# Optimization experiments

Measured on AMD Instinct MI355X. Metric: run time of the kernel, lower is better.

## Reference

```python
import jax, jax.numpy as jnp
import numpy as np

N = 2048      # number of ROIs
C = 1024      # in_channels == inter_channels
G = 16        # groups
D = C // G    # per-group dim = 64


def _bbox_overlaps(b1, b2):
    # mmdet-1.x IoU with +1 pixel convention; b1:(N,4), b2:(M,4)
    area1 = (b1[:, 2] - b1[:, 0] + 1) * (b1[:, 3] - b1[:, 1] + 1)  # (N,)
    area2 = (b2[:, 2] - b2[:, 0] + 1) * (b2[:, 3] - b2[:, 1] + 1)  # (M,)
    lt = jnp.maximum(b1[:, None, :2], b2[None, :, :2])             # (N,M,2)
    rb = jnp.minimum(b1[:, None, 2:], b2[None, :, 2:])             # (N,M,2)
    wh = jnp.clip(rb - lt + 1, 0)
    inter = wh[..., 0] * wh[..., 1]                                # (N,M)
    return inter / (area1[:, None] + area2[None, :] - inter)


def setup_inputs() -> dict:
    key = jax.random.key(0)
    ks = jax.random.split(key, 9)
    in_x = jax.random.normal(ks[0], (N, C), dtype=jnp.float32)
    # valid boxes: [batch_idx, x1, y1, x2, y2]
    xy = jax.random.uniform(ks[1], (N, 2), minval=0.0, maxval=800.0)
    wh = jax.random.uniform(ks[2], (N, 2), minval=8.0, maxval=200.0)
    rois = jnp.concatenate([jnp.zeros((N, 1)), xy, xy + wh], axis=1).astype(jnp.float32)
    s = 1.0 / np.sqrt(C)
    W0 = jax.random.normal(ks[3], (C, C), dtype=jnp.float32) * s
    b0 = jnp.zeros((C,), dtype=jnp.float32)
    W1 = jax.random.normal(ks[4], (C, C), dtype=jnp.float32) * s
    b1 = jnp.zeros((C,), dtype=jnp.float32)
    # grouped 1x1 conv: per group maps C channels -> D channels
    Wout = jax.random.normal(ks[5], (G, D, C), dtype=jnp.float32) * s
    bout = jnp.zeros((C,), dtype=jnp.float32)
    return {"in_x": in_x, "rois": rois, "W0": W0, "b0": b0, "W1": W1,
            "b1": b1, "Wout": Wout, "bout": bout}


def reference(in_x, rois, W0, b0, W1, b1, Wout, bout):
    # self-attention path: in_ref_x = in_x, ref_rois = rois
    # embed convs are pre-activation (relu -> 1x1 conv), shared for x and ref_x
    def embed(v):
        v = jax.nn.relu(v) @ W0.T + b0
        v = jax.nn.relu(v) @ W1.T + b1
        return v
    x = embed(in_x)                      # (N, C)
    ref_x = x                            # shared convs, same input
    xg = x.reshape(N, G, D)
    rg = ref_x.reshape(N, G, D)
    scores = jnp.einsum('ngd,mgd->ngm', xg, rg) / jnp.sqrt(jnp.float32(D))  # (N,G,N)
    ious = _bbox_overlaps(rois[:, 1:], rois[:, 1:])                          # (N,N)
    scores = scores + jnp.log(ious[:, None, :] + 1e-6)
    attn = jax.nn.softmax(scores, axis=2)                                    # (N,G,N)
    y = jnp.einsum('ngm,mc->ngc', attn, in_x)                                # (N,G,C)
    out = jnp.einsum('ngc,goc->ngo', y, Wout).reshape(N, C) + bout           # (N,C)
    return out
```

## Files before the change

### kernel.cpp

```cpp
#include <hip/hip_runtime.h>
#include <math.h>

constexpr int NROI = 2048;
constexpr int CDIM = 1024;
constexpr int NG   = 16;
constexpr int DH   = 64;

typedef __attribute__((ext_vector_type(8))) short short8;
typedef __attribute__((ext_vector_type(4))) float floatx4;

#define MFMA_BF16(a, b, c) __builtin_amdgcn_mfma_f32_16x16x32_bf16((a), (b), (c), 0, 0, 0)

__device__ __forceinline__ short f2bf(float f) {
  unsigned u = __float_as_uint(f);
  unsigned r = 0x7fffu + ((u >> 16) & 1u);
  return (short)((u + r) >> 16);
}
__device__ __forceinline__ unsigned pack2(float a, float b) {
  return (unsigned)(unsigned short)f2bf(a) | ((unsigned)(unsigned short)f2bf(b) << 16);
}

typedef __attribute__((address_space(1))) void GV;
typedef __attribute__((address_space(3))) void LV;
__device__ __forceinline__ void gl2lds16(const void* g, void* l) {
  __builtin_amdgcn_global_load_lds((GV*)g, (LV*)l, 16, 0, 0);
}

__device__ __forceinline__ short8 brelu(short8 v) {
  union { short8 s; unsigned u[4]; } x; x.s = v;
#pragma unroll
  for (int i = 0; i < 4; ++i) {
    unsigned m = (x.u[i] >> 15) & 0x10001u;
    x.u[i] &= ~(m * 0xFFFFu);
  }
  return x.s;
}

__global__ __launch_bounds__(256) void convert_kernel(
    const float* __restrict__ in_x, const float* __restrict__ W0,
    const float* __restrict__ W1, const float* __restrict__ Wout,
    short* __restrict__ xin_b, short* __restrict__ W0b,
    short* __restrict__ W1b, short* __restrict__ Woutb)
{
  const int i = blockIdx.x * 256 + threadIdx.x;
  {
    const float4 v = ((const float4*)in_x)[i];
    uint2 u; u.x = pack2(v.x, v.y); u.y = pack2(v.z, v.w);
    ((uint2*)xin_b)[i] = u;
  }
  if (i < 262144) {
    float4 v = ((const float4*)W0)[i];
    uint2 u; u.x = pack2(v.x, v.y); u.y = pack2(v.z, v.w);
    ((uint2*)W0b)[i] = u;
    v = ((const float4*)W1)[i];
    u.x = pack2(v.x, v.y); u.y = pack2(v.z, v.w);
    ((uint2*)W1b)[i] = u;
    v = ((const float4*)Wout)[i];
    u.x = pack2(v.x, v.y); u.y = pack2(v.z, v.w);
    ((uint2*)Woutb)[i] = u;
  }
}

__global__ __launch_bounds__(256) void iou_kernel(const float* __restrict__ rois,
                                                  unsigned short* __restrict__ biasb)
{
  const int q = blockIdx.y;
  const int k = blockIdx.x * 256 + threadIdx.x;
  const float qx1 = rois[q * 5 + 1], qy1 = rois[q * 5 + 2];
  const float qx2 = rois[q * 5 + 3], qy2 = rois[q * 5 + 4];
  const float qa = (qx2 - qx1 + 1.f) * (qy2 - qy1 + 1.f);
  const float kx1 = rois[k * 5 + 1], ky1 = rois[k * 5 + 2];
  const float kx2 = rois[k * 5 + 3], ky2 = rois[k * 5 + 4];
  const float ka = (kx2 - kx1 + 1.f) * (ky2 - ky1 + 1.f);
  float iw = fminf(qx2, kx2) - fmaxf(qx1, kx1) + 1.f;
  float ih = fminf(qy2, ky2) - fmaxf(qy1, ky1) + 1.f;
  iw = fmaxf(iw, 0.f); ih = fmaxf(ih, 0.f);
  const float inter = iw * ih;
  const float iou = inter / (qa + ka - inter);
  biasb[(size_t)q * NROI + k] = (unsigned short)f2bf(iou + 1e-6f);
}

__global__ __launch_bounds__(256) void gemm_fusedA(
    const short* __restrict__ A, const short* __restrict__ BW0,
    const short* __restrict__ BWout, const float* __restrict__ b0,
    short* __restrict__ t0b, short* __restrict__ zT)
{
  __shared__ short As[8 * 512];
  __shared__ short Bs[8 * 512];
  const int isW0 = blockIdx.x < 16;
  const int col0 = (blockIdx.x & 15) * 64;
  const short* B = isW0 ? BW0 : BWout;
  const int t = threadIdx.x, w = t >> 6, lane = t & 63;
  const int wm = w >> 1, wn = w & 1;
  const int row0 = blockIdx.y * 64;
  const int rlo = lane & 15, khi = (lane >> 4) * 8;

  floatx4 acc[2][2];
#pragma unroll
  for (int i = 0; i < 2; ++i)
#pragma unroll
    for (int j = 0; j < 2; ++j) acc[i][j] = (floatx4){0.f, 0.f, 0.f, 0.f};

  for (int k0 = 0; k0 < CDIM; k0 += 64) {
    __syncthreads();
#pragma unroll
    for (int kh = 0; kh < 2; ++kh) {
      gl2lds16(A + (size_t)(row0 + w * 16 + rlo) * CDIM + k0 + kh * 32 + khi,
               &As[(w * 2 + kh) * 512]);
      gl2lds16(B + (size_t)(col0 + w * 16 + rlo) * CDIM + k0 + kh * 32 + khi,
               &Bs[(w * 2 + kh) * 512]);
    }
    __syncthreads();
#pragma unroll
    for (int kh = 0; kh < 2; ++kh) {
      short8 a0 = *(const short8*)&As[((wm * 2 + 0) * 2 + kh) * 512 + lane * 8];
      short8 a1 = *(const short8*)&As[((wm * 2 + 1) * 2 + kh) * 512 + lane * 8];
      if (isW0) { a0 = brelu(a0); a1 = brelu(a1); }
      const short8 b0f = *(const short8*)&Bs[((wn * 2 + 0) * 2 + kh) * 512 + lane * 8];
      const short8 b1f = *(const short8*)&Bs[((wn * 2 + 1) * 2 + kh) * 512 + lane * 8];
      acc[0][0] = MFMA_BF16(a0, b0f, acc[0][0]);
      acc[0][1] = MFMA_BF16(a0, b1f, acc[0][1]);
      acc[1][0] = MFMA_BF16(a1, b0f, acc[1][0]);
      acc[1][1] = MFMA_BF16(a1, b1f, acc[1][1]);
    }
  }

  const int colL = lane & 15, qq = lane >> 4;
  float bj[2] = {0.f, 0.f};
  if (isW0) {
    bj[0] = b0[col0 + wn * 32 + colL];
    bj[1] = b0[col0 + wn * 32 + 16 + colL];
  }
#pragma unroll
  for (int i = 0; i < 2; ++i)
#pragma unroll
    for (int j = 0; j < 2; ++j)
#pragma unroll
      for (int r = 0; r < 4; ++r) {
        const int row = row0 + wm * 32 + i * 16 + qq * 4 + r;
        const int cc  = col0 + wn * 32 + j * 16 + colL;
        const short bv = f2bf(acc[i][j][r] + bj[j]);
        if (isW0) t0b[(size_t)row * CDIM + cc] = bv;
        else      zT[(size_t)cc * NROI + row] = bv;
      }
}

__global__ __launch_bounds__(256) void gemm_relu_nt(
    const short* __restrict__ A, const short* __restrict__ B,
    const float* __restrict__ bias, short* __restrict__ C)
{
  __shared__ short As[8 * 512];
  __shared__ short Bs[8 * 512];
  const int t = threadIdx.x, w = t >> 6, lane = t & 63;
  const int wm = w >> 1, wn = w & 1;
  const int row0 = blockIdx.y * 64, col0 = blockIdx.x * 64;
  const int rlo = lane & 15, khi = (lane >> 4) * 8;

  floatx4 acc[2][2];
#pragma unroll
  for (int i = 0; i < 2; ++i)
#pragma unroll
    for (int j = 0; j < 2; ++j) acc[i][j] = (floatx4){0.f, 0.f, 0.f, 0.f};

  for (int k0 = 0; k0 < CDIM; k0 += 64) {
    __syncthreads();
#pragma unroll
    for (int kh = 0; kh < 2; ++kh) {
      gl2lds16(A + (size_t)(row0 + w * 16 + rlo) * CDIM + k0 + kh * 32 + khi,
               &As[(w * 2 + kh) * 512]);
      gl2lds16(B + (size_t)(col0 + w * 16 + rlo) * CDIM + k0 + kh * 32 + khi,
               &Bs[(w * 2 + kh) * 512]);
    }
    __syncthreads();
#pragma unroll
    for (int kh = 0; kh < 2; ++kh) {
      short8 a0 = *(const short8*)&As[((wm * 2 + 0) * 2 + kh) * 512 + lane * 8];
      short8 a1 = *(const short8*)&As[((wm * 2 + 1) * 2 + kh) * 512 + lane * 8];
      a0 = brelu(a0); a1 = brelu(a1);
      const short8 b0f = *(const short8*)&Bs[((wn * 2 + 0) * 2 + kh) * 512 + lane * 8];
      const short8 b1f = *(const short8*)&Bs[((wn * 2 + 1) * 2 + kh) * 512 + lane * 8];
      acc[0][0] = MFMA_BF16(a0, b0f, acc[0][0]);
      acc[0][1] = MFMA_BF16(a0, b1f, acc[0][1]);
      acc[1][0] = MFMA_BF16(a1, b0f, acc[1][0]);
      acc[1][1] = MFMA_BF16(a1, b1f, acc[1][1]);
    }
  }

  const int colL = lane & 15, qq = lane >> 4;
  float bj[2];
  bj[0] = bias[col0 + wn * 32 + colL];
  bj[1] = bias[col0 + wn * 32 + 16 + colL];
#pragma unroll
  for (int i = 0; i < 2; ++i)
#pragma unroll
    for (int j = 0; j < 2; ++j)
#pragma unroll
      for (int r = 0; r < 4; ++r) {
        const int row = row0 + wm * 32 + i * 16 + qq * 4 + r;
        const int cc  = col0 + wn * 32 + j * 16 + colL;
        C[(size_t)row * CDIM + cc] = f2bf(acc[i][j][r] + bj[j]);
      }
}

__global__ __launch_bounds__(512) void attn_split(
    const short* __restrict__ Xb,
    const short* __restrict__ ZTb,
    const unsigned short* __restrict__ biasb,
    float* __restrict__ O0, short* __restrict__ O1,
    float* __restrict__ lsums)
{
  const int g  = blockIdx.y;
  const int n0 = blockIdx.x * 128;
  const int sp = blockIdx.z;
  const int mbase = sp * 1024;
  const int t = threadIdx.x, w = t >> 6, lane = t & 63;
  const int col = lane & 15, qq = lane >> 4;
  const int t16 = (w >> 1) * 16, h32 = (w & 1) * 32;
  const int rlo = lane & 15, khi = (lane >> 4) * 8;

  __shared__ short Kf[2][8 * 512];
  __shared__ short Vf[2][8 * 512];
  __shared__ short Pf[8 * 1024];

  const size_t qoff = (size_t)(n0 + w * 16 + col) * CDIM + g * DH;
  const short8 qf0 = *(const short8*)(Xb + qoff + qq * 8);
  const short8 qf1 = *(const short8*)(Xb + qoff + 32 + qq * 8);

  floatx4 oc[4];
#pragma unroll
  for (int dt = 0; dt < 4; ++dt) oc[dt] = (floatx4){0.f, 0.f, 0.f, 0.f};
  float lsum[4] = {0.f, 0.f, 0.f, 0.f};

  const int qrow0 = n0 + w * 16 + qq * 4;

  uint2 bbc[4], bbn[4];
#pragma unroll
  for (int ct = 0; ct < 4; ++ct)
    bbc[ct] = *(const uint2*)(biasb + (size_t)(mbase + ct * 16 + col) * NROI + qrow0);

  gl2lds16(Xb + (size_t)(mbase + t16 + rlo) * CDIM + g * DH + h32 + khi, &Kf[0][w * 512]);
  gl2lds16(ZTb + (size_t)(g * DH + t16 + rlo) * NROI + mbase + h32 + khi, &Vf[0][w * 512]);
  __syncthreads();

  for (int it = 0; it < 16; ++it) {
    const int p = it & 1;
    if (it < 15) {
      const int m1 = mbase + (it + 1) * 64;
      gl2lds16(Xb + (size_t)(m1 + t16 + rlo) * CDIM + g * DH + h32 + khi,
               &Kf[1 - p][w * 512]);
      gl2lds16(ZTb + (size_t)(g * DH + t16 + rlo) * NROI + m1 + h32 + khi,
               &Vf[1 - p][w * 512]);
#pragma unroll
      for (int ct = 0; ct < 4; ++ct)
        bbn[ct] = *(const uint2*)(biasb + (size_t)(m1 + ct * 16 + col) * NROI + qrow0);
    }

    floatx4 sc[4];
#pragma unroll
    for (int ct = 0; ct < 4; ++ct) {
      const short8 b0 = *(const short8*)&Kf[p][(ct * 2 + 0) * 512 + lane * 8];
      const short8 b1 = *(const short8*)&Kf[p][(ct * 2 + 1) * 512 + lane * 8];
      floatx4 z4 = (floatx4){0.f, 0.f, 0.f, 0.f};
      z4 = MFMA_BF16(qf0, b0, z4);
      z4 = MFMA_BF16(qf1, b1, z4);
      sc[ct] = z4;
    }

#pragma unroll
    for (int ct = 0; ct < 4; ++ct) {
      const unsigned ux = bbc[ct].x, uy = bbc[ct].y;
      sc[ct][0] = __expf(sc[ct][0] * 0.125f) * __uint_as_float(ux << 16);
      sc[ct][1] = __expf(sc[ct][1] * 0.125f) * __uint_as_float(ux & 0xFFFF0000u);
      sc[ct][2] = __expf(sc[ct][2] * 0.125f) * __uint_as_float(uy << 16);
      sc[ct][3] = __expf(sc[ct][3] * 0.125f) * __uint_as_float(uy & 0xFFFF0000u);
    }
#pragma unroll
    for (int r = 0; r < 4; ++r)
      lsum[r] += sc[0][r] + sc[1][r] + sc[2][r] + sc[3][r];

    {
      short* pw = &Pf[w * 1024];
#pragma unroll
      for (int ct = 0; ct < 4; ++ct) {
        const int key = ct * 16 + col;
        const int base = (key >> 5) * 512 + (key & 7);
#pragma unroll
        for (int r = 0; r < 4; ++r) {
          const int dl = (4 * qq + r) + ((key >> 3) & 3) * 16;
          pw[base + dl * 8] = f2bf(sc[ct][r]);
        }
      }
      const short8 pa0 = *(const short8*)&pw[0 * 512 + lane * 8];
      const short8 pa1 = *(const short8*)&pw[1 * 512 + lane * 8];
#pragma unroll
      for (int dt = 0; dt < 4; ++dt) {
        const short8 v0 = *(const short8*)&Vf[p][(dt * 2 + 0) * 512 + lane * 8];
        const short8 v1 = *(const short8*)&Vf[p][(dt * 2 + 1) * 512 + lane * 8];
        oc[dt] = MFMA_BF16(pa0, v0, oc[dt]);
        oc[dt] = MFMA_BF16(pa1, v1, oc[dt]);
      }
    }
    __syncthreads();
#pragma unroll
    for (int ct = 0; ct < 4; ++ct) bbc[ct] = bbn[ct];
  }

#pragma unroll
  for (int r = 0; r < 4; ++r) {
    float s = lsum[r];
    s += __shfl_xor(s, 1); s += __shfl_xor(s, 2);
    s += __shfl_xor(s, 4); s += __shfl_xor(s, 8);
    lsum[r] = s;
  }
  if (col == 0) {
#pragma unroll
    for (int r = 0; r < 4; ++r)
      lsums[sp * (NG * NROI) + g * NROI + qrow0 + r] = lsum[r];
  }
  if (sp == 0) {
#pragma unroll
    for (int dt = 0; dt < 4; ++dt)
#pragma unroll
      for (int r = 0; r < 4; ++r)
        O0[(size_t)(qrow0 + r) * CDIM + g * DH + dt * 16 + col] = oc[dt][r];
  } else {
#pragma unroll
    for (int dt = 0; dt < 4; ++dt)
#pragma unroll
      for (int r = 0; r < 4; ++r)
        O1[(size_t)(qrow0 + r) * CDIM + g * DH + dt * 16 + col] = f2bf(oc[dt][r]);
  }
}

__global__ __launch_bounds__(256) void merge_kernel(
    const float* __restrict__ O0, const short* __restrict__ O1,
    const float* __restrict__ lsums, const float* __restrict__ bout,
    float* __restrict__ Out)
{
  const int i = blockIdx.x * 256 + threadIdx.x;
  const int base = i * 4, q = base >> 10, c = base & 1023, g = c >> 6;
  const float l = lsums[g * NROI + q] + lsums[NG * NROI + g * NROI + q];
  const float linv = 1.f / l;
  const float4 o0 = ((const float4*)O0)[i];
  const uint2 o1 = ((const uint2*)O1)[i];
  const float4 bo = *(const float4*)(bout + c);
  float4 o;
  o.x = (o0.x + __uint_as_float(o1.x << 16))          * linv + bo.x;
  o.y = (o0.y + __uint_as_float(o1.x & 0xFFFF0000u))  * linv + bo.y;
  o.z = (o0.z + __uint_as_float(o1.y << 16))          * linv + bo.z;
  o.w = (o0.w + __uint_as_float(o1.y & 0xFFFF0000u))  * linv + bo.w;
  ((float4*)Out)[i] = o;
}

extern "C" void kernel_launch(void* const* d_in, const int* in_sizes, int n_in,
                              void* d_out, int out_size, void* d_ws, size_t ws_size,
                              hipStream_t stream) {
  const float* in_x = (const float*)d_in[0];
  const float* rois = (const float*)d_in[1];
  const float* W0   = (const float*)d_in[2];
  const float* b0   = (const float*)d_in[3];
  const float* W1   = (const float*)d_in[4];
  const float* b1   = (const float*)d_in[5];
  const float* Wout = (const float*)d_in[6];
  const float* bout = (const float*)d_in[7];
  char* w8 = (char*)d_ws;

  short* xin_b = (short*)w8;
  short* W0b   = (short*)(w8 + (4u << 20));
  short* Woutb = (short*)(w8 + (6u << 20));
  unsigned short* biasb = (unsigned short*)(w8 + (4u << 20));
  short* zT    = (short*)(w8 + (12u << 20));
  short* O1    = (short*)(w8 + (16u << 20));
  short* W1b   = (short*)(w8 + (20u << 20));
  float* lsums = (float*)(w8 + (20u << 20));
  short* xb  = xin_b;
  short* t0b = (short*)d_out;
  float* O0  = (float*)d_out;

  convert_kernel<<<2048, 256, 0, stream>>>(in_x, W0, W1, Wout,
                                           xin_b, W0b, W1b, Woutb);
  gemm_fusedA<<<dim3(32, 32), 256, 0, stream>>>(xin_b, W0b, Woutb, b0, t0b, zT);
  iou_kernel<<<dim3(NROI / 256, NROI), 256, 0, stream>>>(rois, biasb);
  gemm_relu_nt<<<dim3(16, 32), 256, 0, stream>>>(t0b, W1b, b1, xb);
  attn_split<<<dim3(NROI / 128, NG, 2), 512, 0, stream>>>(xb, zT, biasb, O0, O1, lsums);
  merge_kernel<<<2048, 256, 0, stream>>>(O0, O1, lsums, bout, (float*)d_out);
}
```

Before: 201.1 us.

## Fuse IoU into convert, enlarge first GEMM tiles, drop attention split and merge

The IoU computation is folded into the conversion kernel and now stores log(iou) in bf16, so the attention exponent becomes a single fmaf+exp. The first GEMM moves from 64x64 to 128x128 tiles, and the transposed Wout-projection stores are packed into 64-bit writes. The attention kernel no longer splits the key range into two halves: it loops over all 2048 keys, normalizes and adds the bias in its own epilogue, and the merge kernel is removed. This saves launches and the intermediate O0/O1/lsum traffic, but halves the attention grid (256 blocks), which can lower occupancy on a many-CU device. It also quantizes P with truncation instead of rounding.

```diff
diff --git a/kernel.cpp b/kernel.cpp
--- a/kernel.cpp
+++ b/kernel.cpp
@@ -16,6 +16,9 @@
   unsigned r = 0x7fffu + ((u >> 16) & 1u);
   return (short)((u + r) >> 16);
 }
+__device__ __forceinline__ short f2bf_rtz(float f) {
+  return (short)(__float_as_uint(f) >> 16);
+}
 __device__ __forceinline__ unsigned pack2(float a, float b) {
   return (unsigned)(unsigned short)f2bf(a) | ((unsigned)(unsigned short)f2bf(b) << 16);
 }
@@ -36,113 +39,132 @@
   return x.s;
 }
 
-__global__ __launch_bounds__(256) void convert_kernel(
+__global__ __launch_bounds__(256) void conv_iou(
     const float* __restrict__ in_x, const float* __restrict__ W0,
     const float* __restrict__ W1, const float* __restrict__ Wout,
+    const float* __restrict__ rois,
     short* __restrict__ xin_b, short* __restrict__ W0b,
-    short* __restrict__ W1b, short* __restrict__ Woutb)
+    short* __restrict__ W1b, short* __restrict__ Woutb,
+    unsigned short* __restrict__ biasln)
 {
-  const int i = blockIdx.x * 256 + threadIdx.x;
-  {
-    const float4 v = ((const float4*)in_x)[i];
-    uint2 u; u.x = pack2(v.x, v.y); u.y = pack2(v.z, v.w);
-    ((uint2*)xin_b)[i] = u;
-  }
-  if (i < 262144) {
-    float4 v = ((const float4*)W0)[i];
-    uint2 u; u.x = pack2(v.x, v.y); u.y = pack2(v.z, v.w);
-    ((uint2*)W0b)[i] = u;
-    v = ((const float4*)W1)[i];
-    u.x = pack2(v.x, v.y); u.y = pack2(v.z, v.w);
-    ((uint2*)W1b)[i] = u;
-    v = ((const float4*)Wout)[i];
-    u.x = pack2(v.x, v.y); u.y = pack2(v.z, v.w);
-    ((uint2*)Woutb)[i] = u;
-  }
-}
-
-__global__ __launch_bounds__(256) void iou_kernel(const float* __restrict__ rois,
-                                                  unsigned short* __restrict__ biasb)
-{
-  const int q = blockIdx.y;
-  const int k = blockIdx.x * 256 + threadIdx.x;
-  const float qx1 = rois[q * 5 + 1], qy1 = rois[q * 5 + 2];
-  const float qx2 = rois[q * 5 + 3], qy2 = rois[q * 5 + 4];
-  const float qa = (qx2 - qx1 + 1.f) * (qy2 - qy1 + 1.f);
-  const float kx1 = rois[k * 5 + 1], ky1 = rois[k * 5 + 2];
-  const float kx2 = rois[k * 5 + 3], ky2 = rois[k * 5 + 4];
-  const float ka = (kx2 - kx1 + 1.f) * (ky2 - ky1 + 1.f);
-  float iw = fminf(qx2, kx2) - fmaxf(qx1, kx1) + 1.f;
-  float ih = fminf(qy2, ky2) - fmaxf(qy1, ky1) + 1.f;
-  iw = fmaxf(iw, 0.f); ih = fmaxf(ih, 0.f);
-  const float inter = iw * ih;
-  const float iou = inter / (qa + ka - inter);
-  biasb[(size_t)q * NROI + k] = (unsigned short)f2bf(iou + 1e-6f);
-}
-
-__global__ __launch_bounds__(256) void gemm_fusedA(
+  const int b = blockIdx.x;
+  if (b < 2048) {
+    const int i = b * 256 + threadIdx.x;
+    {
+      const float4 v = ((const float4*)in_x)[i];
+      uint2 u; u.x = pack2(v.x, v.y); u.y = pack2(v.z, v.w);
+      ((uint2*)xin_b)[i] = u;
+    }
+    if (i < 262144) {
+      float4 v = ((const float4*)W0)[i];
+      uint2 u; u.x = pack2(v.x, v.y); u.y = pack2(v.z, v.w);
+      ((uint2*)W0b)[i] = u;
+      v = ((const float4*)W1)[i];
+      u.x = pack2(v.x, v.y); u.y = pack2(v.z, v.w);
+      ((uint2*)W1b)[i] = u;
+      v = ((const float4*)Wout)[i];
+      u.x = pack2(v.x, v.y); u.y = pack2(v.z, v.w);
+      ((uint2*)Woutb)[i] = u;
+    }
+  } else {
+    const int p = (b - 2048) * 256 + threadIdx.x;
+    const int q = p >> 11, k = p & 2047;
+    const float qx1 = rois[q * 5 + 1], qy1 = rois[q * 5 + 2];
+    const float qx2 = rois[q * 5 + 3], qy2 = rois[q * 5 + 4];
+    const float qa = (qx2 - qx1 + 1.f) * (qy2 - qy1 + 1.f);
+    const float kx1 = rois[k * 5 + 1], ky1 = rois[k * 5 + 2];
+    const float kx2 = rois[k * 5 + 3], ky2 = rois[k * 5 + 4];
+    const float ka = (kx2 - kx1 + 1.f) * (ky2 - ky1 + 1.f);
+    float iw = fminf(qx2, kx2) - fmaxf(qx1, kx1) + 1.f;
+    float ih = fminf(qy2, ky2) - fmaxf(qy1, ky1) + 1.f;
+    iw = fmaxf(iw, 0.f); ih = fmaxf(ih, 0.f);
+    const float inter = iw * ih;
+    const float iou = inter / (qa + ka - inter);
+    biasln[p] = (unsigned short)f2bf(__logf(iou + 1e-6f));
+  }
+}
+
+__global__ __launch_bounds__(256) void gemm128(
     const short* __restrict__ A, const short* __restrict__ BW0,
     const short* __restrict__ BWout, const float* __restrict__ b0,
     short* __restrict__ t0b, short* __restrict__ zT)
 {
-  __shared__ short As[8 * 512];
-  __shared__ short Bs[8 * 512];
-  const int isW0 = blockIdx.x < 16;
-  const int col0 = (blockIdx.x & 15) * 64;
-  const short* B = isW0 ? BW0 : BWout;
+  __shared__ short As[16 * 512];
+  __shared__ short Bs[16 * 512];
   const int t = threadIdx.x, w = t >> 6, lane = t & 63;
   const int wm = w >> 1, wn = w & 1;
-  const int row0 = blockIdx.y * 64;
-  const int rlo = lane & 15, khi = (lane >> 4) * 8;
-
-  floatx4 acc[2][2];
-#pragma unroll
-  for (int i = 0; i < 2; ++i)
-#pragma unroll
-    for (int j = 0; j < 2; ++j) acc[i][j] = (floatx4){0.f, 0.f, 0.f, 0.f};
+  const int row0 = blockIdx.y * 128;
+  const int col0g = blockIdx.x * 128;
+  const int isW0 = col0g < 1024;
+  const short* B = isW0 ? BW0 : BWout;
+  const int col0 = col0g & 1023;
+  const int srow = lane & 15, skq = (lane >> 4) * 8;
+
+  floatx4 acc[4][4];
+#pragma unroll
+  for (int i = 0; i < 4; ++i)
+#pragma unroll
+    for (int j = 0; j < 4; ++j) acc[i][j] = (floatx4){0.f, 0.f, 0.f, 0.f};
 
   for (int k0 = 0; k0 < CDIM; k0 += 64) {
     __syncthreads();
 #pragma unroll
+    for (int q = 0; q < 4; ++q) {
+      const int f = w * 4 + q, rt = f >> 1, kh = f & 1;
+      gl2lds16(A + (size_t)(row0 + rt * 16 + srow) * CDIM + k0 + kh * 32 + skq,
+               &As[f * 512]);
+      gl2lds16(B + (size_t)(col0 + rt * 16 + srow) * CDIM + k0 + kh * 32 + skq,
+               &Bs[f * 512]);
+    }
+    __syncthreads();
+#pragma unroll
     for (int kh = 0; kh < 2; ++kh) {
-      gl2lds16(A + (size_t)(row0 + w * 16 + rlo) * CDIM + k0 + kh * 32 + khi,
-               &As[(w * 2 + kh) * 512]);
-      gl2lds16(B + (size_t)(col0 + w * 16 + rlo) * CDIM + k0 + kh * 32 + khi,
-               &Bs[(w * 2 + kh) * 512]);
-    }
-    __syncthreads();
-#pragma unroll
-    for (int kh = 0; kh < 2; ++kh) {
-      short8 a0 = *(const short8*)&As[((wm * 2 + 0) * 2 + kh) * 512 + lane * 8];
-      short8 a1 = *(const short8*)&As[((wm * 2 + 1) * 2 + kh) * 512 + lane * 8];
-      if (isW0) { a0 = brelu(a0); a1 = brelu(a1); }
-      const short8 b0f = *(const short8*)&Bs[((wn * 2 + 0) * 2 + kh) * 512 + lane * 8];
-      const short8 b1f = *(const short8*)&Bs[((wn * 2 + 1) * 2 + kh) * 512 + lane * 8];
-      acc[0][0] = MFMA_BF16(a0, b0f, acc[0][0]);
-      acc[0][1] = MFMA_BF16(a0, b1f, acc[0][1]);
-      acc[1][0] = MFMA_BF16(a1, b0f, acc[1][0]);
-      acc[1][1] = MFMA_BF16(a1, b1f, acc[1][1]);
+      short8 a[4], bf[4];
+#pragma unroll
+      for (int i = 0; i < 4; ++i) {
+        a[i] = *(const short8*)&As[(((wm * 4 + i) * 2) + kh) * 512 + lane * 8];
+        if (isW0) a[i] = brelu(a[i]);
+      }
+#pragma unroll
+      for (int j = 0; j < 4; ++j)
+        bf[j] = *(const short8*)&Bs[(((wn * 4 + j) * 2) + kh) * 512 + lane * 8];
+#pragma unroll
+      for (int i = 0; i < 4; ++i)
+#pragma unroll
+        for (int j = 0; j < 4; ++j)
+          acc[i][j] = MFMA_BF16(a[i], bf[j], acc[i][j]);
     }
   }
 
   const int colL = lane & 15, qq = lane >> 4;
-  float bj[2] = {0.f, 0.f};
   if (isW0) {
-    bj[0] = b0[col0 + wn * 32 + colL];
-    bj[1] = b0[col0 + wn * 32 + 16 + colL];
-  }
-#pragma unroll
-  for (int i = 0; i < 2; ++i)
-#pragma unroll
-    for (int j = 0; j < 2; ++j)
-#pragma unroll
-      for (int r = 0; r < 4; ++r) {
-        const int row = row0 + wm * 32 + i * 16 + qq * 4 + r;
-        const int cc  = col0 + wn * 32 + j * 16 + colL;
-        const short bv = f2bf(acc[i][j][r] + bj[j]);
-        if (isW0) t0b[(size_t)row * CDIM + cc] = bv;
-        else      zT[(size_t)cc * NROI + row] = bv;
-      }
+    float bj[4];
+#pragma unroll
+    for (int j = 0; j < 4; ++j) bj[j] = b0[col0 + wn * 64 + j * 16 + colL];
+#pragma unroll
+    for (int i = 0; i < 4; ++i)
+#pragma unroll
+      for (int j = 0; j < 4; ++j)
+#pragma unroll
+        for (int r = 0; r < 4; ++r) {
+          const int row = row0 + wm * 64 + i * 16 + qq * 4 + r;
+          const int cc  = col0 + wn * 64 + j * 16 + colL;
+          t0b[(size_t)row * CDIM + cc] = f2bf(acc[i][j][r] + bj[j]);
+        }
+  } else {
+#pragma unroll
+    for (int i = 0; i < 4; ++i)
+#pragma unroll
+      for (int j = 0; j < 4; ++j) {
+        unsigned long long u = 0;
+#pragma unroll
+        for (int r = 0; r < 4; ++r)
+          u |= ((unsigned long long)(unsigned short)f2bf(acc[i][j][r])) << (16 * r);
+        const int cc  = col0 + wn * 64 + j * 16 + colL;
+        const int row = row0 + wm * 64 + i * 16 + qq * 4;
+        *(unsigned long long*)&zT[(size_t)cc * NROI + row] = u;
+      }
+  }
 }
 
 __global__ __launch_bounds__(256) void gemm_relu_nt(
@@ -202,17 +224,15 @@
       }
 }
 
-__global__ __launch_bounds__(512) void attn_split(
+__global__ __launch_bounds__(512) void attn_ln(
     const short* __restrict__ Xb,
     const short* __restrict__ ZTb,
-    const unsigned short* __restrict__ biasb,
-    float* __restrict__ O0, short* __restrict__ O1,
-    float* __restrict__ lsums)
+    const unsigned short* __restrict__ biasln,
+    const float* __restrict__ bout,
+    float* __restrict__ Out)
 {
   const int g  = blockIdx.y;
   const int n0 = blockIdx.x * 128;
-  const int sp = blockIdx.z;
-  const int mbase = sp * 1024;
   const int t = threadIdx.x, w = t >> 6, lane = t & 63;
   const int col = lane & 15, qq = lane >> 4;
   const int t16 = (w >> 1) * 16, h32 = (w & 1) * 32;
@@ -236,23 +256,24 @@
   uint2 bbc[4], bbn[4];
 #pragma unroll
   for (int ct = 0; ct < 4; ++ct)
-    bbc[ct] = *(const uint2*)(biasb + (size_t)(mbase + ct * 16 + col) * NROI + qrow0);
-
-  gl2lds16(Xb + (size_t)(mbase + t16 + rlo) * CDIM + g * DH + h32 + khi, &Kf[0][w * 512]);
-  gl2lds16(ZTb + (size_t)(g * DH + t16 + rlo) * NROI + mbase + h32 + khi, &Vf[0][w * 512]);
+    bbc[ct] = *(const uint2*)(biasln + (size_t)(ct * 16 + col) * NROI + qrow0);
+
+  gl2lds16(Xb + (size_t)(t16 + rlo) * CDIM + g * DH + h32 + khi, &Kf[0][w * 512]);
+  gl2lds16(ZTb + (size_t)(g * DH + t16 + rlo) * NROI + h32 + khi, &Vf[0][w * 512]);
   __syncthreads();
 
-  for (int it = 0; it < 16; ++it) {
+  for (int it = 0; it < NROI / 64; ++it) {
     const int p = it & 1;
-    if (it < 15) {
-      const int m1 = mbase + (it + 1) * 64;
+    const int m0 = it * 64;
+    if (it + 1 < NROI / 64) {
+      const int m1 = m0 + 64;
       gl2lds16(Xb + (size_t)(m1 + t16 + rlo) * CDIM + g * DH + h32 + khi,
                &Kf[1 - p][w * 512]);
       gl2lds16(ZTb + (size_t)(g * DH + t16 + rlo) * NROI + m1 + h32 + khi,
                &Vf[1 - p][w * 512]);
 #pragma unroll
       for (int ct = 0; ct < 4; ++ct)
-        bbn[ct] = *(const uint2*)(biasb + (size_t)(m1 + ct * 16 + col) * NROI + qrow0);
+        bbn[ct] = *(const uint2*)(biasln + (size_t)(m1 + ct * 16 + col) * NROI + qrow0);
     }
 
     floatx4 sc[4];
@@ -269,10 +290,10 @@
 #pragma unroll
     for (int ct = 0; ct < 4; ++ct) {
       const unsigned ux = bbc[ct].x, uy = bbc[ct].y;
-      sc[ct][0] = __expf(sc[ct][0] * 0.125f) * __uint_as_float(ux << 16);
-      sc[ct][1] = __expf(sc[ct][1] * 0.125f) * __uint_as_float(ux & 0xFFFF0000u);
-      sc[ct][2] = __expf(sc[ct][2] * 0.125f) * __uint_as_float(uy << 16);
-      sc[ct][3] = __expf(sc[ct][3] * 0.125f) * __uint_as_float(uy & 0xFFFF0000u);
+      sc[ct][0] = __expf(fmaf(sc[ct][0], 0.125f, __uint_as_float(ux << 16)));
+      sc[ct][1] = __expf(fmaf(sc[ct][1], 0.125f, __uint_as_float(ux & 0xFFFF0000u)));
+      sc[ct][2] = __expf(fmaf(sc[ct][2], 0.125f, __uint_as_float(uy << 16)));
+      sc[ct][3] = __expf(fmaf(sc[ct][3], 0.125f, __uint_as_float(uy & 0xFFFF0000u)));
     }
 #pragma unroll
     for (int r = 0; r < 4; ++r)
@@ -287,7 +308,7 @@
 #pragma unroll
         for (int r = 0; r < 4; ++r) {
           const int dl = (4 * qq + r) + ((key >> 3) & 3) * 16;
-          pw[base + dl * 8] = f2bf(sc[ct][r]);
+          pw[base + dl * 8] = f2bf_rtz(sc[ct][r]);
         }
       }
       const short8 pa0 = *(const short8*)&pw[0 * 512 + lane * 8];
@@ -312,44 +333,14 @@
     s += __shfl_xor(s, 4); s += __shfl_xor(s, 8);
     lsum[r] = s;
   }
-  if (col == 0) {
+#pragma unroll
+  for (int dt = 0; dt < 4; ++dt) {
+    const float bo = bout[g * DH + dt * 16 + col];
 #pragma unroll
     for (int r = 0; r < 4; ++r)
-      lsums[sp * (NG * NROI) + g * NROI + qrow0 + r] = lsum[r];
-  }
-  if (sp == 0) {
-#pragma unroll
-    for (int dt = 0; dt < 4; ++dt)
-#pragma unroll
-      for (int r = 0; r < 4; ++r)
-        O0[(size_t)(qrow0 + r) * CDIM + g * DH + dt * 16 + col] = oc[dt][r];
-  } else {
-#pragma unroll
-    for (int dt = 0; dt < 4; ++dt)
-#pragma unroll
-      for (int r = 0; r < 4; ++r)
-        O1[(size_t)(qrow0 + r) * CDIM + g * DH + dt * 16 + col] = f2bf(oc[dt][r]);
-  }
-}
-
-__global__ __launch_bounds__(256) void merge_kernel(
-    const float* __restrict__ O0, const short* __restrict__ O1,
-    const float* __restrict__ lsums, const float* __restrict__ bout,
-    float* __restrict__ Out)
-{
-  const int i = blockIdx.x * 256 + threadIdx.x;
-  const int base = i * 4, q = base >> 10, c = base & 1023, g = c >> 6;
-  const float l = lsums[g * NROI + q] + lsums[NG * NROI + g * NROI + q];
-  const float linv = 1.f / l;
-  const float4 o0 = ((const float4*)O0)[i];
-  const uint2 o1 = ((const uint2*)O1)[i];
-  const float4 bo = *(const float4*)(bout + c);
-  float4 o;
-  o.x = (o0.x + __uint_as_float(o1.x << 16))          * linv + bo.x;
-  o.y = (o0.y + __uint_as_float(o1.x & 0xFFFF0000u))  * linv + bo.y;
-  o.z = (o0.z + __uint_as_float(o1.y << 16))          * linv + bo.z;
-  o.w = (o0.w + __uint_as_float(o1.y & 0xFFFF0000u))  * linv + bo.w;
-  ((float4*)Out)[i] = o;
+      Out[(size_t)(qrow0 + r) * CDIM + g * DH + dt * 16 + col] =
+          oc[dt][r] / lsum[r] + bo;
+  }
 }
 
 extern "C" void kernel_launch(void* const* d_in, const int* in_sizes, int n_in,
@@ -366,22 +357,18 @@
   char* w8 = (char*)d_ws;
 
   short* xin_b = (short*)w8;
-  short* W0b   = (short*)(w8 + (4u << 20));
-  short* Woutb = (short*)(w8 + (6u << 20));
-  unsigned short* biasb = (unsigned short*)(w8 + (4u << 20));
-  short* zT    = (short*)(w8 + (12u << 20));
-  short* O1    = (short*)(w8 + (16u << 20));
-  short* W1b   = (short*)(w8 + (20u << 20));
-  float* lsums = (float*)(w8 + (20u << 20));
+  short* W0b   = (short*)(w8 + ((size_t)4 << 20));
+  short* W1b   = (short*)(w8 + ((size_t)6 << 20));
+  short* Woutb = (short*)(w8 + ((size_t)8 << 20));
+  short* zT    = (short*)(w8 + ((size_t)10 << 20));
+  unsigned short* biasln = (unsigned short*)(w8 + ((size_t)14 << 20));
   short* xb  = xin_b;
   short* t0b = (short*)d_out;
-  float* O0  = (float*)d_out;
-
-  convert_kernel<<<2048, 256, 0, stream>>>(in_x, W0, W1, Wout,
-                                           xin_b, W0b, W1b, Woutb);
-  gemm_fusedA<<<dim3(32, 32), 256, 0, stream>>>(xin_b, W0b, Woutb, b0, t0b, zT);
-  iou_kernel<<<dim3(NROI / 256, NROI), 256, 0, stream>>>(rois, biasb);
+
+  conv_iou<<<2048 + 16384, 256, 0, stream>>>(in_x, W0, W1, Wout, rois,
+                                             xin_b, W0b, W1b, Woutb, biasln);
+  gemm128<<<dim3(16, 16), 256, 0, stream>>>(xin_b, W0b, Woutb, b0, t0b, zT);
   gemm_relu_nt<<<dim3(16, 32), 256, 0, stream>>>(t0b, W1b, b1, xb);
-  attn_split<<<dim3(NROI / 128, NG, 2), 512, 0, stream>>>(xb, zT, biasb, O0, O1, lsums);
-  merge_kernel<<<2048, 256, 0, stream>>>(O0, O1, lsums, bout, (float*)d_out);
-}
+  attn_ln<<<dim3(NROI / 128, NG), 512, 0, stream>>>(xb, zT, biasln, bout,
+                                                    (float*)d_out);
+}
```

Result: slower. 205.5 us (+2.2%).
